# Performance work log

Measured on AMD Instinct MI355X. Metric: run time of the kernel, lower is better.

Reference implementation:

```python
import jax, jax.numpy as jnp
import numpy as np

EPS = 1e-6

def _phi(x):
    # elu(x) + 1 feature map
    return jax.nn.elu(x) + 1.0

def setup_inputs() -> dict:
    key = jax.random.key(0)
    kq, kk, kv = jax.random.split(key, 3)
    N, L, S, H, D, M = 8, 4096, 4096, 8, 64, 64
    queries = jax.random.normal(kq, (N, L, H, D), dtype=jnp.float32)
    keys = jax.random.normal(kk, (N, S, H, D), dtype=jnp.float32)
    values = jax.random.normal(kv, (N, S, H, M), dtype=jnp.float32)
    key_mask = jnp.ones((N, S), dtype=jnp.float32)  # key_lengths.float_matrix
    return {"queries": queries, "keys": keys, "values": values, "key_mask": key_mask}

def reference(queries, keys, values, key_mask):
    Q = _phi(queries)                                   # [N,L,H,D]
    K = _phi(keys) * key_mask[:, :, None, None]         # [N,S,H,D]
    KV = jnp.einsum('nshd,nshm->nhmd', K, values)       # [N,H,M,D]
    Z = 1.0 / (jnp.einsum('nlhd,nhd->nlh', Q, K.sum(axis=1)) + EPS)  # [N,L,H]
    V = jnp.einsum('nlhd,nhmd,nlh->nlhm', Q, KV, Z)     # [N,L,H,M]
    return V
```

## Files before the change

kernel.cpp:

```cpp
#include <hip/hip_runtime.h>


#define SLEN 4096
#define LLEN 4096
#define NHTOT 64
#define HD   512
#define NSPLIT 16
#define EPSF 1e-6f

typedef short s16x8 __attribute__((ext_vector_type(8)));
typedef float f32x4 __attribute__((ext_vector_type(4)));

__device__ __forceinline__ float phi(float x) {
    return x > 0.0f ? x + 1.0f : __expf(x);
}

__device__ __forceinline__ unsigned pack_hi2(float a, float b) {
    return (__float_as_uint(a) >> 16) | (__float_as_uint(b) & 0xFFFF0000u);
}
__device__ __forceinline__ float bres(float x) {
    return x - __uint_as_float(__float_as_uint(x) & 0xFFFF0000u);
}
__device__ __forceinline__ void bsplit(float x, short& hi, short& lo) {
    const unsigned bx = __float_as_uint(x);
    hi = (short)(bx >> 16);
    const float hf = __uint_as_float(bx & 0xFFFF0000u);
    lo = (short)(__float_as_uint(x - hf) >> 16);
}

__global__ __launch_bounds__(256, 4)
void la_phase1(const float* __restrict__ Kg, const float* __restrict__ Vg,
               const float* __restrict__ maskg,
               float* __restrict__ KVp, float* __restrict__ Ksump) {
    __shared__ char  sb[2][16384];
    __shared__ float ksb[8 * 64];

    const int tid  = threadIdx.x;
    const int w    = tid >> 6;
    const int lane = tid & 63;
    const int nh   = blockIdx.y;
    const int n    = nh >> 3;
    const int h    = nh & 7;
    const int sp   = blockIdx.x;

    const bool isK = (w < 2);
    const int idx  = tid & 127;
    const int c    = idx & 15;
    const int q    = idx >> 4;
    const int c4   = c * 4;
    const float* __restrict__ src = isK ? Kg : Vg;
    const int arro = isK ? 0 : 8192;
    const int woff = (((q >> 1) ^ (c & 3)) << 4) | ((q & 1) << 3);

    const int wd = w & 1, wm = w >> 1;
    const int r  = lane & 15, a = lane >> 4;
    const int cho = ((a ^ ((r >> 2) & 3)) << 4);

    const size_t base = (size_t)n * SLEN * HD + (size_t)h * 64;
    const float* mrow = maskg + (size_t)n * SLEN;
    const int brow0 = sp * 256;

    f32x4 acc[2][2];
    #pragma unroll
    for (int dt = 0; dt < 2; ++dt)
        #pragma unroll
        for (int mt = 0; mt < 2; ++mt)
            acc[dt][mt] = (f32x4){0.f, 0.f, 0.f, 0.f};
    float4 ksp = make_float4(0.f, 0.f, 0.f, 0.f);

    float4 p[4];
    float  pm[4];
    #pragma unroll
    for (int j = 0; j < 4; ++j) {
        const int s = brow0 + q * 4 + j;
        p[j] = *(const float4*)(src + base + (size_t)s * HD + c4);
        if (isK) pm[j] = mrow[s];
    }

    #pragma unroll 2
    for (int t = 0; t < 8; ++t) {
        char* bb = &sb[t & 1][arro];
        float4 vv[4];
        if (isK) {
            #pragma unroll
            for (int j = 0; j < 4; ++j) {
                float4 kq = p[j];
                const float mm = pm[j];
                kq.x = phi(kq.x) * mm; kq.y = phi(kq.y) * mm;
                kq.z = phi(kq.z) * mm; kq.w = phi(kq.w) * mm;
                ksp.x += kq.x; ksp.y += kq.y; ksp.z += kq.z; ksp.w += kq.w;
                vv[j] = kq;
            }
        } else {
            #pragma unroll
            for (int j = 0; j < 4; ++j) vv[j] = p[j];
        }
        #pragma unroll
        for (int i = 0; i < 4; ++i) {
            const int doff = (c4 + i) * 64 + woff;
            const float x0 = (&vv[0].x)[i], x1 = (&vv[1].x)[i];
            const float x2 = (&vv[2].x)[i], x3 = (&vv[3].x)[i];
            *(uint2*)(bb + doff)        = make_uint2(pack_hi2(x0, x1), pack_hi2(x2, x3));
            *(uint2*)(bb + 4096 + doff) = make_uint2(pack_hi2(bres(x0), bres(x1)),
                                                     pack_hi2(bres(x2), bres(x3)));
        }
        __syncthreads();

        if (t < 7) {
            #pragma unroll
            for (int j = 0; j < 4; ++j) {
                const int s = brow0 + (t + 1) * 32 + q * 4 + j;
                p[j] = *(const float4*)(src + base + (size_t)s * HD + c4);
                if (isK) pm[j] = mrow[s];
            }
        }

        const char* rbK = &sb[t & 1][0];
        const char* rbV = &sb[t & 1][8192];
        s16x8 Ah[2], Al[2], Bh[2], Bl[2];
        #pragma unroll
        for (int dt = 0; dt < 2; ++dt) {
            const int off = ((wd * 2 + dt) * 16 + r) * 64 + cho;
            Ah[dt] = *(const s16x8*)(rbK + off);
            Al[dt] = *(const s16x8*)(rbK + 4096 + off);
        }
        #pragma unroll
        for (int mt = 0; mt < 2; ++mt) {
            const int off = ((wm * 2 + mt) * 16 + r) * 64 + cho;
            Bh[mt] = *(const s16x8*)(rbV + off);
            Bl[mt] = *(const s16x8*)(rbV + 4096 + off);
        }
        #pragma unroll
        for (int dt = 0; dt < 2; ++dt)
            #pragma unroll
            for (int mt = 0; mt < 2; ++mt) {
                acc[dt][mt] = __builtin_amdgcn_mfma_f32_16x16x32_bf16(Ah[dt], Bh[mt], acc[dt][mt], 0, 0, 0);
                acc[dt][mt] = __builtin_amdgcn_mfma_f32_16x16x32_bf16(Ah[dt], Bl[mt], acc[dt][mt], 0, 0, 0);
                acc[dt][mt] = __builtin_amdgcn_mfma_f32_16x16x32_bf16(Al[dt], Bh[mt], acc[dt][mt], 0, 0, 0);
            }
    }

    if (isK) *(float4*)&ksb[q * 64 + c4] = ksp;
    __syncthreads();
    if (tid < 64) {
        float ssum = 0.f;
        #pragma unroll
        for (int rr = 0; rr < 8; ++rr) ssum += ksb[rr * 64 + tid];
        Ksump[((size_t)sp * NHTOT + nh) * 64 + tid] = ssum;
    }

    float* outp = KVp + ((size_t)sp * NHTOT + nh) * 4096;
    #pragma unroll
    for (int dt = 0; dt < 2; ++dt)
        #pragma unroll
        for (int mt = 0; mt < 2; ++mt)
            #pragma unroll
            for (int pp = 0; pp < 4; ++pp)
                outp[(wd * 32 + dt * 16 + a * 4 + pp) * 64 + wm * 32 + mt * 16 + r] = acc[dt][mt][pp];
}

__global__ __launch_bounds__(256)
void la_reduce(const float* __restrict__ KVp, const float* __restrict__ Ksump,
               short* __restrict__ KVThi, short* __restrict__ KVTlo,
               float* __restrict__ Ksum) {
    __shared__ float ld[64 * 20];

    const int nh  = blockIdx.y;
    const int mb  = blockIdx.x * 16;
    const int tid = threadIdx.x;

    const int d    = tid >> 2;
    const int moff = (tid & 3) * 4;
    float4 a = make_float4(0.f, 0.f, 0.f, 0.f);
    #pragma unroll
    for (int s = 0; s < NSPLIT; ++s) {
        const float4 v = *(const float4*)&KVp[((size_t)s * NHTOT + nh) * 4096 + d * 64 + mb + moff];
        a.x += v.x; a.y += v.y; a.z += v.z; a.w += v.w;
    }
    *(float4*)&ld[d * 20 + moff] = a;
    __syncthreads();

    const int mloc = tid >> 4;
    const int d0   = (tid & 15) * 4;
    short hi4[4], lo4[4];
    #pragma unroll
    for (int i = 0; i < 4; ++i)
        bsplit(ld[(d0 + i) * 20 + mloc], hi4[i], lo4[i]);
    const size_t o = (size_t)nh * 4096 + (mb + mloc) * 64 + d0;
    *(short4*)&KVThi[o] = *(short4*)hi4;
    *(short4*)&KVTlo[o] = *(short4*)lo4;

    if (blockIdx.x == 0 && tid < 64) {
        float b = 0.f;
        #pragma unroll
        for (int s = 0; s < NSPLIT; ++s)
            b += Ksump[((size_t)s * NHTOT + nh) * 64 + tid];
        Ksum[nh * 64 + tid] = b;
    }
}

__global__ __launch_bounds__(256)
void la_phase2(const float* __restrict__ Qg,
               const short* __restrict__ KVThi, const short* __restrict__ KVTlo,
               const float* __restrict__ Ksum, float* __restrict__ Og) {
    const int tid  = threadIdx.x;
    const int w    = tid >> 6;
    const int lane = tid & 63;
    const int nh   = blockIdx.y;
    const int n    = nh >> 3;
    const int h    = nh & 7;
    const int l0   = blockIdx.x * 128 + w * 32;

    const int r  = lane & 15;
    const int g4 = lane >> 4;

    const short* bhp = KVThi + (size_t)nh * 4096;
    const short* blp = KVTlo + (size_t)nh * 4096;
    const float* ksp = Ksum + nh * 64;

    f32x4 acc[2][4];
    #pragma unroll
    for (int t = 0; t < 2; ++t)
        #pragma unroll
        for (int u = 0; u < 4; ++u)
            acc[t][u] = (f32x4){0.f, 0.f, 0.f, 0.f};
    float den[2] = {0.f, 0.f};

    #pragma unroll
    for (int g = 0; g < 2; ++g) {
        const int db = g * 32 + g4 * 8;

        s16x8 Bh[4], Bl[4];
        #pragma unroll
        for (int u = 0; u < 4; ++u) {
            Bh[u] = *(const s16x8*)&bhp[(u * 16 + r) * 64 + db];
            Bl[u] = *(const s16x8*)&blp[(u * 16 + r) * 64 + db];
        }
        const float4 k0 = *(const float4*)&ksp[db];
        const float4 k1 = *(const float4*)&ksp[db + 4];

        #pragma unroll
        for (int t = 0; t < 2; ++t) {
            const float* qrow = Qg + ((size_t)(n * LLEN + l0 + t * 16 + r) * 8 + h) * 64 + db;
            float4 q0 = *(const float4*)qrow;
            float4 q1 = *(const float4*)(qrow + 4);
            q0.x = phi(q0.x); q0.y = phi(q0.y); q0.z = phi(q0.z); q0.w = phi(q0.w);
            q1.x = phi(q1.x); q1.y = phi(q1.y); q1.z = phi(q1.z); q1.w = phi(q1.w);

            float dn = den[t];
            dn = fmaf(q0.x, k0.x, dn); dn = fmaf(q0.y, k0.y, dn);
            dn = fmaf(q0.z, k0.z, dn); dn = fmaf(q0.w, k0.w, dn);
            dn = fmaf(q1.x, k1.x, dn); dn = fmaf(q1.y, k1.y, dn);
            dn = fmaf(q1.z, k1.z, dn); dn = fmaf(q1.w, k1.w, dn);
            den[t] = dn;

            s16x8 Ah, Al;
            {
                short hh, ll;
                bsplit(q0.x, hh, ll); Ah[0] = hh; Al[0] = ll;
                bsplit(q0.y, hh, ll); Ah[1] = hh; Al[1] = ll;
                bsplit(q0.z, hh, ll); Ah[2] = hh; Al[2] = ll;
                bsplit(q0.w, hh, ll); Ah[3] = hh; Al[3] = ll;
                bsplit(q1.x, hh, ll); Ah[4] = hh; Al[4] = ll;
                bsplit(q1.y, hh, ll); Ah[5] = hh; Al[5] = ll;
                bsplit(q1.z, hh, ll); Ah[6] = hh; Al[6] = ll;
                bsplit(q1.w, hh, ll); Ah[7] = hh; Al[7] = ll;
            }
            #pragma unroll
            for (int u = 0; u < 4; ++u) {
                acc[t][u] = __builtin_amdgcn_mfma_f32_16x16x32_bf16(Ah, Bh[u], acc[t][u], 0, 0, 0);
                acc[t][u] = __builtin_amdgcn_mfma_f32_16x16x32_bf16(Ah, Bl[u], acc[t][u], 0, 0, 0);
                acc[t][u] = __builtin_amdgcn_mfma_f32_16x16x32_bf16(Al, Bh[u], acc[t][u], 0, 0, 0);
            }
        }
    }

    #pragma unroll
    for (int t = 0; t < 2; ++t) {
        den[t] += __shfl_xor(den[t], 16, 64);
        den[t] += __shfl_xor(den[t], 32, 64);
    }

    #pragma unroll
    for (int t = 0; t < 2; ++t) {
        #pragma unroll
        for (int k = 0; k < 4; ++k) {
            const int ro = g4 * 4 + k;
            const float dk = __shfl(den[t], ro, 64);
            const float z  = 1.0f / (dk + EPSF);
            const int l = l0 + t * 16 + ro;
            float* op = &Og[((size_t)(n * LLEN + l) * 8 + h) * 64 + r];
            #pragma unroll
            for (int u = 0; u < 4; ++u)
                op[u * 16] = acc[t][u][k] * z;
        }
    }
}

extern "C" void kernel_launch(void* const* d_in, const int* in_sizes, int n_in,
                              void* d_out, int out_size, void* d_ws, size_t ws_size,
                              hipStream_t stream) {
    const float* Q    = (const float*)d_in[0];
    const float* K    = (const float*)d_in[1];
    const float* V    = (const float*)d_in[2];
    const float* mask = (const float*)d_in[3];
    float* out = (float*)d_out;

    float* KVp   = (float*)d_ws;
    float* Ksump = KVp + (size_t)NSPLIT * NHTOT * 4096;
    float* Ksum  = Ksump + (size_t)NSPLIT * NHTOT * 64;
    short* KVThi = (short*)(Ksum + NHTOT * 64);
    short* KVTlo = KVThi + (size_t)NHTOT * 4096;

    dim3 g1(NSPLIT, NHTOT);
    la_phase1<<<g1, 256, 0, stream>>>(K, V, mask, KVp, Ksump);

    dim3 gr(4, NHTOT);
    la_reduce<<<gr, 256, 0, stream>>>(KVp, Ksump, KVThi, KVTlo, Ksum);

    dim3 g2(LLEN / 128, NHTOT);
    la_phase2<<<g2, 256, 0, stream>>>(Q, KVThi, KVTlo, Ksum, out);
}
```

Before: 244.6 us.

## Deepen phase1 load pipeline to two tiles ahead and pad LDS rows

```diff
diff --git a/kernel.cpp b/kernel.cpp
--- a/kernel.cpp
+++ b/kernel.cpp
@@ -8,6 +8,10 @@
 #define NSPLIT 16
 #define EPSF 1e-6f
 
+#define ROWB 72
+#define ARRB 4608
+#define BUFB 18432
+
 typedef short s16x8 __attribute__((ext_vector_type(8)));
 typedef float f32x4 __attribute__((ext_vector_type(4)));
 
@@ -32,7 +36,7 @@
 void la_phase1(const float* __restrict__ Kg, const float* __restrict__ Vg,
                const float* __restrict__ maskg,
                float* __restrict__ KVp, float* __restrict__ Ksump) {
-    __shared__ char  sb[2][16384];
+    __shared__ char  sb[2][BUFB];
     __shared__ float ksb[8 * 64];
 
     const int tid  = threadIdx.x;
@@ -49,12 +53,10 @@
     const int q    = idx >> 4;
     const int c4   = c * 4;
     const float* __restrict__ src = isK ? Kg : Vg;
-    const int arro = isK ? 0 : 8192;
-    const int woff = (((q >> 1) ^ (c & 3)) << 4) | ((q & 1) << 3);
+    const int arro = isK ? 0 : 2 * ARRB;
 
     const int wd = w & 1, wm = w >> 1;
     const int r  = lane & 15, a = lane >> 4;
-    const int cho = ((a ^ ((r >> 2) & 3)) << 4);
 
     const size_t base = (size_t)n * SLEN * HD + (size_t)h * 64;
     const float* mrow = maskg + (size_t)n * SLEN;
@@ -68,76 +70,96 @@
             acc[dt][mt] = (f32x4){0.f, 0.f, 0.f, 0.f};
     float4 ksp = make_float4(0.f, 0.f, 0.f, 0.f);
 
-    float4 p[4];
-    float  pm[4];
-    #pragma unroll
-    for (int j = 0; j < 4; ++j) {
-        const int s = brow0 + q * 4 + j;
-        p[j] = *(const float4*)(src + base + (size_t)s * HD + c4);
-        if (isK) pm[j] = mrow[s];
-    }
-
-    #pragma unroll 2
-    for (int t = 0; t < 8; ++t) {
-        char* bb = &sb[t & 1][arro];
-        float4 vv[4];
-        if (isK) {
-            #pragma unroll
-            for (int j = 0; j < 4; ++j) {
-                float4 kq = p[j];
-                const float mm = pm[j];
-                kq.x = phi(kq.x) * mm; kq.y = phi(kq.y) * mm;
-                kq.z = phi(kq.z) * mm; kq.w = phi(kq.w) * mm;
-                ksp.x += kq.x; ksp.y += kq.y; ksp.z += kq.z; ksp.w += kq.w;
-                vv[j] = kq;
-            }
-        } else {
-            #pragma unroll
-            for (int j = 0; j < 4; ++j) vv[j] = p[j];
-        }
-        #pragma unroll
-        for (int i = 0; i < 4; ++i) {
-            const int doff = (c4 + i) * 64 + woff;
-            const float x0 = (&vv[0].x)[i], x1 = (&vv[1].x)[i];
-            const float x2 = (&vv[2].x)[i], x3 = (&vv[3].x)[i];
-            *(uint2*)(bb + doff)        = make_uint2(pack_hi2(x0, x1), pack_hi2(x2, x3));
-            *(uint2*)(bb + 4096 + doff) = make_uint2(pack_hi2(bres(x0), bres(x1)),
-                                                     pack_hi2(bres(x2), bres(x3)));
-        }
-        __syncthreads();
-
-        if (t < 7) {
-            #pragma unroll
-            for (int j = 0; j < 4; ++j) {
-                const int s = brow0 + (t + 1) * 32 + q * 4 + j;
-                p[j] = *(const float4*)(src + base + (size_t)s * HD + c4);
-                if (isK) pm[j] = mrow[s];
-            }
-        }
-
-        const char* rbK = &sb[t & 1][0];
-        const char* rbV = &sb[t & 1][8192];
-        s16x8 Ah[2], Al[2], Bh[2], Bl[2];
-        #pragma unroll
-        for (int dt = 0; dt < 2; ++dt) {
-            const int off = ((wd * 2 + dt) * 16 + r) * 64 + cho;
-            Ah[dt] = *(const s16x8*)(rbK + off);
-            Al[dt] = *(const s16x8*)(rbK + 4096 + off);
-        }
-        #pragma unroll
-        for (int mt = 0; mt < 2; ++mt) {
-            const int off = ((wm * 2 + mt) * 16 + r) * 64 + cho;
-            Bh[mt] = *(const s16x8*)(rbV + off);
-            Bl[mt] = *(const s16x8*)(rbV + 4096 + off);
-        }
-        #pragma unroll
-        for (int dt = 0; dt < 2; ++dt)
-            #pragma unroll
-            for (int mt = 0; mt < 2; ++mt) {
-                acc[dt][mt] = __builtin_amdgcn_mfma_f32_16x16x32_bf16(Ah[dt], Bh[mt], acc[dt][mt], 0, 0, 0);
-                acc[dt][mt] = __builtin_amdgcn_mfma_f32_16x16x32_bf16(Ah[dt], Bl[mt], acc[dt][mt], 0, 0, 0);
-                acc[dt][mt] = __builtin_amdgcn_mfma_f32_16x16x32_bf16(Al[dt], Bh[mt], acc[dt][mt], 0, 0, 0);
-            }
+#define LOADSTEP(P, PM, T) do {                                               \
+        _Pragma("unroll")                                                     \
+        for (int j = 0; j < 4; ++j) {                                         \
+            const int s_ = brow0 + (T) * 32 + q * 4 + j;                      \
+            P[j] = *(const float4*)(src + base + (size_t)s_ * HD + c4);       \
+            if (isK) PM[j] = mrow[s_];                                        \
+        }                                                                     \
+    } while (0)
+
+#define STAGESTEP(P, PM, BUF) do {                                            \
+        char* bb_ = &sb[BUF][arro];                                           \
+        float4 vv_[4];                                                        \
+        if (isK) {                                                            \
+            _Pragma("unroll")                                                 \
+            for (int j = 0; j < 4; ++j) {                                     \
+                float4 kq_ = P[j];                                            \
+                const float mm_ = PM[j];                                      \
+                kq_.x = phi(kq_.x) * mm_; kq_.y = phi(kq_.y) * mm_;           \
+                kq_.z = phi(kq_.z) * mm_; kq_.w = phi(kq_.w) * mm_;           \
+                ksp.x += kq_.x; ksp.y += kq_.y;                               \
+                ksp.z += kq_.z; ksp.w += kq_.w;                               \
+                vv_[j] = kq_;                                                 \
+            }                                                                 \
+        } else {                                                              \
+            _Pragma("unroll")                                                 \
+            for (int j = 0; j < 4; ++j) vv_[j] = P[j];                        \
+        }                                                                     \
+        _Pragma("unroll")                                                     \
+        for (int i = 0; i < 4; ++i) {                                         \
+            const int off_ = (c4 + i) * ROWB + q * 8;                         \
+            const float x0_ = (&vv_[0].x)[i], x1_ = (&vv_[1].x)[i];           \
+            const float x2_ = (&vv_[2].x)[i], x3_ = (&vv_[3].x)[i];           \
+            *(uint2*)(bb_ + off_) =                                           \
+                make_uint2(pack_hi2(x0_, x1_), pack_hi2(x2_, x3_));           \
+            *(uint2*)(bb_ + ARRB + off_) =                                    \
+                make_uint2(pack_hi2(bres(x0_), bres(x1_)),                    \
+                           pack_hi2(bres(x2_), bres(x3_)));                   \
+        }                                                                     \
+    } while (0)
+
+#define PIPE_BAR() do {                                                       \
+        asm volatile("s_waitcnt lgkmcnt(0)" ::: "memory");                    \
+        __builtin_amdgcn_s_barrier();                                         \
+        asm volatile("" ::: "memory");                                        \
+    } while (0)
+
+#define COMPSTEP(BUF) do {                                                    \
+        const char* rbK_ = &sb[BUF][0];                                       \
+        const char* rbV_ = &sb[BUF][2 * ARRB];                                \
+        s16x8 Ah_[2], Al_[2], Bh_[2], Bl_[2];                                 \
+        _Pragma("unroll")                                                     \
+        for (int dt = 0; dt < 2; ++dt) {                                      \
+            const int off_ = ((wd * 2 + dt) * 16 + r) * ROWB + a * 16;        \
+            Ah_[dt] = *(const s16x8*)(rbK_ + off_);                           \
+            Al_[dt] = *(const s16x8*)(rbK_ + ARRB + off_);                    \
+        }                                                                     \
+        _Pragma("unroll")                                                     \
+        for (int mt = 0; mt < 2; ++mt) {                                      \
+            const int off_ = ((wm * 2 + mt) * 16 + r) * ROWB + a * 16;        \
+            Bh_[mt] = *(const s16x8*)(rbV_ + off_);                           \
+            Bl_[mt] = *(const s16x8*)(rbV_ + ARRB + off_);                    \
+        }                                                                     \
+        _Pragma("unroll")                                                     \
+        for (int dt = 0; dt < 2; ++dt)                                        \
+            _Pragma("unroll")                                                 \
+            for (int mt = 0; mt < 2; ++mt) {                                  \
+                acc[dt][mt] = __builtin_amdgcn_mfma_f32_16x16x32_bf16(        \
+                    Ah_[dt], Bh_[mt], acc[dt][mt], 0, 0, 0);                  \
+                acc[dt][mt] = __builtin_amdgcn_mfma_f32_16x16x32_bf16(        \
+                    Ah_[dt], Bl_[mt], acc[dt][mt], 0, 0, 0);                  \
+                acc[dt][mt] = __builtin_amdgcn_mfma_f32_16x16x32_bf16(        \
+                    Al_[dt], Bh_[mt], acc[dt][mt], 0, 0, 0);                  \
+            }                                                                 \
+    } while (0)
+
+    float4 pe[4], po[4];
+    float  pme[4], pmo[4];
+    LOADSTEP(pe, pme, 0);
+    LOADSTEP(po, pmo, 1);
+
+    #pragma unroll
+    for (int tt = 0; tt < 4; ++tt) {
+        STAGESTEP(pe, pme, 0);
+        PIPE_BAR();
+        if (tt < 3) LOADSTEP(pe, pme, 2 * tt + 2);
+        COMPSTEP(0);
+        STAGESTEP(po, pmo, 1);
+        PIPE_BAR();
+        if (tt < 3) LOADSTEP(po, pmo, 2 * tt + 3);
+        COMPSTEP(1);
     }
 
     if (isK) *(float4*)&ksb[q * 64 + c4] = ksp;
@@ -157,6 +179,11 @@
             #pragma unroll
             for (int pp = 0; pp < 4; ++pp)
                 outp[(wd * 32 + dt * 16 + a * 4 + pp) * 64 + wm * 32 + mt * 16 + r] = acc[dt][mt][pp];
+
+#undef LOADSTEP
+#undef STAGESTEP
+#undef PIPE_BAR
+#undef COMPSTEP
 }
 
 __global__ __launch_bounds__(256)
```

New measurement: 258.4 us. 5.7% more time.
